# Kernel optimization log

Measured on AMD Instinct MI355X. Metric: run time of the kernel, lower is better.

The kernel has to match this reference:

```python
import jax, jax.numpy as jnp
import numpy as np

B, S, D, H, HD = 2, 2048, 2048, 16, 128
MAX_TIMESCALE = 10000.0


def _fixed_pos_embedding(features, length, max_timescale):
    # flaxformer embedding.generate_fixed_pos_embedding
    fraction = jnp.arange(0, features, 2, dtype=jnp.float32) / features
    timescale = max_timescale ** fraction  # min_timescale = 1.0
    sinusoid = jnp.einsum('i,j->ij', jnp.arange(length, dtype=jnp.float32), 1.0 / timescale)
    sinusoid = jnp.concatenate([sinusoid, sinusoid], axis=-1)  # [length, features]
    return jnp.sin(sinusoid), jnp.cos(sinusoid)


def _rotate_half(x):
    x1, x2 = jnp.split(x, 2, axis=-1)
    return jnp.concatenate([-x2, x1], axis=-1)


def _apply_rope(x, sin, cos):
    # x: [B, S, H, HD]; sin/cos: [S, HD]
    sin = sin[None, :, None, :].astype(x.dtype)
    cos = cos[None, :, None, :].astype(x.dtype)
    return x * cos + _rotate_half(x) * sin


def setup_inputs() -> dict:
    key = jax.random.key(0)
    ks = jax.random.split(key, 6)
    inputs_q = jax.random.normal(ks[0], (B, S, D), dtype=jnp.float32)
    inputs_kv = jax.random.normal(ks[1], (B, S, D), dtype=jnp.float32)
    scale = D ** -0.5
    wq = jax.random.normal(ks[2], (D, H, HD), dtype=jnp.float32) * scale
    wk = jax.random.normal(ks[3], (D, H, HD), dtype=jnp.float32) * scale
    wv = jax.random.normal(ks[4], (D, H, HD), dtype=jnp.float32) * scale
    wo = jax.random.normal(ks[5], (H, HD, D), dtype=jnp.float32) * ((H * HD) ** -0.5)
    mask = jnp.tril(jnp.ones((S, S), dtype=bool))[None, None]  # causal [1,1,S,S]
    return {"inputs_q": inputs_q, "inputs_kv": inputs_kv, "wq": wq, "wk": wk,
            "wv": wv, "wo": wo, "mask": mask}


def reference(inputs_q, inputs_kv, wq, wk, wv, wo, mask):
    # QKV projections (split-head kernels) -> [B, S, H, HD]
    q = jnp.einsum('bqd,dhf->bqhf', inputs_q, wq)
    k = jnp.einsum('bkd,dhf->bkhf', inputs_kv, wk)
    v = jnp.einsum('bkd,dhf->bkhf', inputs_kv, wv)

    # Rotary embeddings applied to full head dim (fraction_to_rotate = 1.0)
    sin, cos = _fixed_pos_embedding(HD, S, MAX_TIMESCALE)
    q = _apply_rope(q, sin, cos)
    k = _apply_rope(k, sin, cos)

    # Logit rescaling by 1/sqrt(head_dim) (rescale_logits=False default path)
    q = q * (HD ** -0.5)

    logits = jnp.einsum('bqhf,bkhf->bhqk', q, k)  # [B, H, S, S]
    logits = jnp.where(mask, logits, jnp.asarray(-1e10, logits.dtype))
    probs = jax.nn.softmax(logits, axis=-1)

    ctx = jnp.einsum('bhqk,bkhf->bqhf', probs, v)
    out = jnp.einsum('bqhf,hfd->bqd', ctx, wo)  # output projection
    return out
```

## Files before the change

kernel.cpp:

```cpp
#include <hip/hip_runtime.h>

#define S_LEN 2048
#define NH 16
#define HDIM 128
#define DMODEL 2048

typedef __attribute__((ext_vector_type(8))) short bf16x8;
typedef __attribute__((ext_vector_type(4))) float f32x4;

using gas_cvp = const __attribute__((address_space(1))) void*;
using las_vp  = __attribute__((address_space(3))) void*;

__device__ __forceinline__ unsigned short f2bf(float x) {
  unsigned int u = __builtin_bit_cast(unsigned int, x);
  u += 0x7FFFu + ((u >> 16) & 1u);
  return (unsigned short)(u >> 16);
}
__device__ __forceinline__ float bf2f(unsigned short u) {
  unsigned int x = ((unsigned int)u) << 16;
  return __builtin_bit_cast(float, x);
}
__device__ __forceinline__ unsigned int cvt_pk_bf16(float lo, float hi) {
  unsigned int r;
  asm("v_cvt_pk_bf16_f32 %0, %1, %2" : "=v"(r) : "v"(lo), "v"(hi));
  return r;
}

__global__ __launch_bounds__(256) void cvt_kernel(const float4* __restrict__ in,
                                                  ushort4* __restrict__ out, int n4) {
  int i = blockIdx.x * 256 + threadIdx.x;
  if (i < n4) {
    float4 v = in[i];
    ushort4 r;
    r.x = f2bf(v.x); r.y = f2bf(v.y); r.z = f2bf(v.z); r.w = f2bf(v.w);
    out[i] = r;
  }
}

__global__ __launch_bounds__(256) void sincos_kernel(float2* __restrict__ sc) {
  int i = blockIdx.x * 256 + threadIdx.x;
  int s = i >> 6, j = i & 63;
  float inv_ts = 1.0f / powf(10000.0f, (float)j * (1.0f / 64.0f));
  float ang = (float)s * inv_ts;
  sc[i] = make_float2(sinf(ang), cosf(ang));
}

__global__ __launch_bounds__(256) void rope8_kernel(const unsigned short* __restrict__ XQ,
                                                    const unsigned short* __restrict__ XK,
                                                    const float2* __restrict__ sc,
                                                    unsigned short* __restrict__ outQ,
                                                    unsigned short* __restrict__ outK,
                                                    float qscale) {
  const unsigned short* X = blockIdx.z ? XK : XQ;
  unsigned short* out = blockIdx.z ? outK : outQ;
  float scale = blockIdx.z ? 1.0f : qscale;
  int i = blockIdx.x * 256 + threadIdx.x;
  int m = i >> 7;
  int r = i & 127;
  int h = r >> 3, jb = (r & 7) * 8;
  int s = m & (S_LEN - 1);
  size_t base = (size_t)m * DMODEL + h * HDIM + jb;
  int4 x1 = *(const int4*)(X + base);
  int4 x2 = *(const int4*)(X + base + 64);
  const float2* pp = sc + s * 64 + jb;
  int4 o1, o2;
  int* x1w = (int*)&x1; int* x2w = (int*)&x2;
  int* o1w = (int*)&o1; int* o2w = (int*)&o2;
#pragma unroll
  for (int w = 0; w < 4; w++) {
    float a_lo = bf2f((unsigned short)(x1w[w] & 0xffff));
    float a_hi = bf2f((unsigned short)((unsigned int)x1w[w] >> 16));
    float b_lo = bf2f((unsigned short)(x2w[w] & 0xffff));
    float b_hi = bf2f((unsigned short)((unsigned int)x2w[w] >> 16));
    float2 c0 = pp[w * 2], c1 = pp[w * 2 + 1];
    float r1l = (a_lo * c0.y - b_lo * c0.x) * scale;
    float r1h = (a_hi * c1.y - b_hi * c1.x) * scale;
    float r2l = (b_lo * c0.y + a_lo * c0.x) * scale;
    float r2h = (b_hi * c1.y + a_hi * c1.x) * scale;
    o1w[w] = (int)(cvt_pk_bf16(r1l, r1h));
    o2w[w] = (int)(cvt_pk_bf16(r2l, r2h));
  }
  *(int4*)(out + base) = o1;
  *(int4*)(out + base + 64) = o2;
}

__global__ __launch_bounds__(256) void wtrans4_kernel(const float* __restrict__ w0,
                                                      const float* __restrict__ w1,
                                                      const float* __restrict__ w2,
                                                      const float* __restrict__ w3,
                                                      unsigned short* __restrict__ outb) {
  __shared__ float tile[64][65];
  int z = blockIdx.z;
  const float* in = (z == 0) ? w0 : (z == 1) ? w1 : (z == 2) ? w2 : w3;
  unsigned short* out = outb + (size_t)z * DMODEL * DMODEL;
  int c0 = blockIdx.x * 64, r0 = blockIdx.y * 64;
  int tx = threadIdx.x & 63, ty = threadIdx.x >> 6;
#pragma unroll
  for (int i = 0; i < 16; i++) {
    int r = ty + i * 4;
    tile[r][tx] = in[(size_t)(r0 + r) * DMODEL + c0 + tx];
  }
  __syncthreads();
#pragma unroll
  for (int i = 0; i < 16; i++) {
    int c = ty + i * 4;
    out[(size_t)(c0 + c) * DMODEL + r0 + tx] = f2bf(tile[tx][c]);
  }
}

__global__ __launch_bounds__(256) void vtrans_kernel(const unsigned short* __restrict__ vf,
                                                     unsigned short* __restrict__ Vt) {
  __shared__ unsigned short tile[64][65];
  int z = blockIdx.z; int b = z >> 4, h = z & 15;
  const unsigned short* I = vf + (size_t)b * S_LEN * DMODEL + h * HDIM;
  unsigned short* O = Vt + (size_t)z * HDIM * S_LEN;
  int s0 = blockIdx.y * 64, f0 = blockIdx.x * 64;
  int tx = threadIdx.x & 63, ty = threadIdx.x >> 6;
#pragma unroll
  for (int i = 0; i < 16; i++) {
    int r = ty + i * 4;
    tile[r][tx] = I[(size_t)(s0 + r) * DMODEL + f0 + tx];
  }
  __syncthreads();
#pragma unroll
  for (int i = 0; i < 16; i++) {
    int c = ty + i * 4;
    O[(size_t)(f0 + c) * S_LEN + s0 + tx] = tile[tx][c];
  }
}

template <bool BF16OUT>
__global__ __launch_bounds__(512, 1) void gemmk_kernel(
    const unsigned short* __restrict__ Aq,
    const unsigned short* __restrict__ Akv,
    const unsigned short* __restrict__ W,
    void* __restrict__ Cb) {
  constexpr int M = 4096, N = 2048, K = 2048, NT = K / 64;
  __shared__ char lds[147456];
  int z = blockIdx.z;
  const unsigned short* A = (z == 0) ? Aq : Akv;
  const unsigned short* Bt = W + (size_t)z * N * K;

  int wid = blockIdx.y * 16 + blockIdx.x;
  int nid = (wid & 7) * 32 + (wid >> 3);
  int bn = (nid & 15) * 128, bm = (nid >> 4) * 256;

  int tid = threadIdx.x, wave = tid >> 6, lane = tid & 63;
  int lr = lane & 15, lq = lane >> 4;
  int wr = wave >> 1, wc = wave & 1;

  auto STAGE_U = [&](int t, int buf, int which) {
    int k0 = t * 64;
    const unsigned short* src = (which < 2) ? A : Bt;
    int rbase = (which < 2) ? (bm + which * 128) : bn;
    char* dst0 = lds + buf * 49152 + which * 16384;
#pragma unroll
    for (int i = 0; i < 2; i++) {
      int o = i * 8192 + wave * 1024 + lane * 16;
      int row = o >> 7, colb = o & 127;
      int sc = colb ^ ((row & 7) << 4);
      __builtin_amdgcn_global_load_lds(
          (gas_cvp)(src + (size_t)(rbase + row) * K + k0 + (sc >> 1)),
          (las_vp)(dst0 + i * 8192 + wave * 1024), 16, 0, 0);
    }
  };
  auto LDA = [&](int buf, int m, int kk) -> bf16x8 {
    int row = wr * 64 + m * 16 + lr;
    int half = row >> 7, r = row & 127;
    int byt = r * 128 + (((kk * 4 + lq) ^ (r & 7)) << 4);
    return *(const bf16x8*)(lds + buf * 49152 + half * 16384 + byt);
  };
  auto LDB = [&](int buf, int n, int kk) -> bf16x8 {
    int row = wc * 64 + n * 16 + lr;
    int byt = row * 128 + (((kk * 4 + lq) ^ (row & 7)) << 4);
    return *(const bf16x8*)(lds + buf * 49152 + 32768 + byt);
  };

  f32x4 acc[4][4] = {};
  bf16x8 aA[4][2], bB[4][2];

  auto QUAD = [&](int mg, int ng) {
#pragma unroll
    for (int kk = 0; kk < 2; kk++)
#pragma unroll
      for (int mm = 0; mm < 2; mm++)
#pragma unroll
        for (int nn = 0; nn < 2; nn++)
          acc[mg * 2 + mm][ng * 2 + nn] = __builtin_amdgcn_mfma_f32_16x16x32_bf16(
              aA[mg * 2 + mm][kk], bB[ng * 2 + nn][kk], acc[mg * 2 + mm][ng * 2 + nn], 0, 0, 0);
  };

  auto BODY = [&](int T, int cur, int dst, int mode) {
    __builtin_amdgcn_s_barrier();
    if (mode == 0) {
      STAGE_U(T + 2, dst, 0); STAGE_U(T + 2, dst, 1); STAGE_U(T + 2, dst, 2);
    }
    __builtin_amdgcn_sched_barrier(0);
#pragma unroll
    for (int kk = 0; kk < 2; kk++)
#pragma unroll
      for (int mm = 0; mm < 2; mm++) aA[mm][kk] = LDA(cur, mm, kk);
#pragma unroll
    for (int kk = 0; kk < 2; kk++)
#pragma unroll
      for (int nn = 0; nn < 2; nn++) bB[nn][kk] = LDB(cur, nn, kk);
    __builtin_amdgcn_sched_barrier(0);
#pragma unroll
    for (int kk = 0; kk < 2; kk++)
#pragma unroll
      for (int nn = 0; nn < 2; nn++) bB[2 + nn][kk] = LDB(cur, 2 + nn, kk);
    __builtin_amdgcn_sched_barrier(0);
#pragma unroll
    for (int kk = 0; kk < 2; kk++)
#pragma unroll
      for (int mm = 0; mm < 2; mm++) aA[2 + mm][kk] = LDA(cur, 2 + mm, kk);
    __builtin_amdgcn_sched_barrier(0);

    asm volatile("s_waitcnt lgkmcnt(8)" ::: "memory");
    __builtin_amdgcn_sched_barrier(0);
    __builtin_amdgcn_s_setprio(1);
    QUAD(0, 0);
    __builtin_amdgcn_s_setprio(0);
    asm volatile("s_waitcnt lgkmcnt(4)" ::: "memory");
    __builtin_amdgcn_sched_barrier(0);
    __builtin_amdgcn_s_setprio(1);
    QUAD(0, 1);
    __builtin_amdgcn_s_setprio(0);
    asm volatile("s_waitcnt lgkmcnt(0)" ::: "memory");
    __builtin_amdgcn_sched_barrier(0);
    __builtin_amdgcn_s_setprio(1);
    QUAD(1, 0); QUAD(1, 1);
    __builtin_amdgcn_s_setprio(0);
    if (mode == 0)      asm volatile("s_waitcnt vmcnt(6)" ::: "memory");
    else if (mode == 1) asm volatile("s_waitcnt vmcnt(0)" ::: "memory");
    __builtin_amdgcn_sched_barrier(0);
  };

  STAGE_U(0, 0, 0); STAGE_U(0, 0, 1); STAGE_U(0, 0, 2);
  STAGE_U(1, 1, 0); STAGE_U(1, 1, 1); STAGE_U(1, 1, 2);
  asm volatile("s_waitcnt vmcnt(6)" ::: "memory");
  __builtin_amdgcn_sched_barrier(0);

  int cur = 0;
  for (int T = 0; T < NT - 2; T++) {
    int dst = (cur == 0) ? 2 : cur - 1;
    BODY(T, cur, dst, 0);
    cur = (cur == 2) ? 0 : cur + 1;
  }
  BODY(NT - 2, cur, 0, 1);
  cur = (cur == 2) ? 0 : cur + 1;
  BODY(NT - 1, cur, 0, 2);
  asm volatile("s_waitcnt vmcnt(0) lgkmcnt(0)" ::: "memory");

#pragma unroll
  for (int m = 0; m < 4; m++)
#pragma unroll
    for (int n = 0; n < 4; n++) {
      int row0 = bm + wr * 64 + m * 16 + lq * 4;
      int col = bn + wc * 64 + n * 16 + lr;
      if (BF16OUT) {
        unsigned short* C = (unsigned short*)Cb + (size_t)z * M * N;
#pragma unroll
        for (int r = 0; r < 4; r++)
          C[(size_t)(row0 + r) * N + col] = f2bf(acc[m][n][r]);
      } else {
        float* C = (float*)Cb + (size_t)z * M * N;
#pragma unroll
        for (int r = 0; r < 4; r++)
          C[(size_t)(row0 + r) * N + col] = acc[m][n][r];
      }
    }
}

__global__ __launch_bounds__(512, 1) void attn_kernel(const unsigned short* __restrict__ Qb,
                                                      const unsigned short* __restrict__ Kb,
                                                      const unsigned short* __restrict__ Vt,
                                                      unsigned short* __restrict__ ctx) {
  __shared__ char lds[65536];
  int d = blockIdx.x + 8 * (blockIdx.y + 16 * blockIdx.z);
  int jlo = (d >> 3) & 7;
  int hb = (d & 7) * 4 + (d >> 6);
  int h = hb & 15, b = hb >> 4;

  int tid = threadIdx.x, wave = tid >> 6, lane = tid & 63;
  int lr = lane & 15, lq = lane >> 4;
  int grp = wave >> 2, wsub = wave & 3;
  int qtile = grp ? (15 - jlo) : jlo;
  int qw = qtile * 128 + wsub * 32;
  int nt = 2 * (15 - jlo) + 2;

  const unsigned short* Qp = Qb + (size_t)b * S_LEN * DMODEL + (size_t)h * HDIM;
  const unsigned short* Kp = Kb + (size_t)b * S_LEN * DMODEL + (size_t)h * HDIM;
  const unsigned short* Vp = Vt + (size_t)(b * NH + h) * HDIM * S_LEN;

  bf16x8 qa[2][4];
#pragma unroll
  for (int mi = 0; mi < 2; mi++)
#pragma unroll
    for (int kf = 0; kf < 4; kf++)
      qa[mi][kf] = *(const bf16x8*)(Qp + (size_t)(qw + mi * 16 + lr) * DMODEL + kf * 32 + lq * 8);

  f32x4 o[2][8] = {};
  float mrow[2] = {-1e30f, -1e30f};
  float lsum[2] = {0.f, 0.f};

  auto STAGE = [&](int tt, int bsel) {
    int kk0 = tt * 64;
#pragma unroll
    for (int i = 0; i < 2; i++) {
      int o_ = wave * 2048 + i * 1024 + lane * 16;
      int row = o_ >> 8, colb = o_ & 255;
      int sc_ = colb ^ ((row & 7) << 4);
      __builtin_amdgcn_global_load_lds(
          (gas_cvp)(Kp + (size_t)(kk0 + row) * DMODEL + (sc_ >> 1)),
          (las_vp)(lds + bsel * 32768 + wave * 2048 + i * 1024), 16, 0, 0);
    }
#pragma unroll
    for (int i = 0; i < 2; i++) {
      int o_ = wave * 2048 + i * 1024 + lane * 16;
      int row = o_ >> 7, colb = o_ & 127;
      int sc_ = colb ^ ((row & 7) << 4);
      __builtin_amdgcn_global_load_lds(
          (gas_cvp)(Vp + (size_t)row * S_LEN + kk0 + (sc_ >> 1)),
          (las_vp)(lds + bsel * 32768 + 16384 + wave * 2048 + i * 1024), 16, 0, 0);
    }
  };

  STAGE(0, 0);
  __syncthreads();

  for (int t = 0; t < nt; t++) {
    int cur = t & 1;
    int k0 = t * 64;
    if (t + 1 < nt) STAGE(t + 1, cur ^ 1);

    bool active = (k0 <= qw + 31);
    if (active) {
      const char* kbb = lds + cur * 32768;
      f32x4 sf[2][4] = {};
#pragma unroll
      for (int kf = 0; kf < 4; kf++) {
        bf16x8 kbf[4];
#pragma unroll
        for (int nf = 0; nf < 4; nf++) {
          int row = nf * 16 + lr;
          int colb = kf * 64 + lq * 16;
          kbf[nf] = *(const bf16x8*)(kbb + row * 256 + (colb ^ ((row & 7) << 4)));
        }
#pragma unroll
        for (int nf = 0; nf < 4; nf++)
#pragma unroll
          for (int mi = 0; mi < 2; mi++)
            sf[mi][nf] = __builtin_amdgcn_mfma_f32_16x16x32_bf16(kbf[nf], qa[mi][kf], sf[mi][nf], 0, 0, 0);
      }

      if (k0 + 63 > qw) {
#pragma unroll
        for (int mi = 0; mi < 2; mi++) {
          int q = qw + mi * 16 + lr;
#pragma unroll
          for (int nf = 0; nf < 4; nf++)
#pragma unroll
            for (int r = 0; r < 4; r++)
              if (k0 + nf * 16 + lq * 4 + r > q) sf[mi][nf][r] = -1e30f;
        }
      }

      float vmax[2];
#pragma unroll
      for (int mi = 0; mi < 2; mi++) {
        float v = sf[mi][0][0];
#pragma unroll
        for (int nf = 0; nf < 4; nf++)
#pragma unroll
          for (int r = 0; r < 4; r++) v = fmaxf(v, sf[mi][nf][r]);
        v = fmaxf(v, __shfl_xor(v, 16));
        v = fmaxf(v, __shfl_xor(v, 32));
        vmax[mi] = v;
      }
      bool need = (vmax[0] > mrow[0] + 8.f) || (vmax[1] > mrow[1] + 8.f);
      if (__any(need)) {
#pragma unroll
        for (int mi = 0; mi < 2; mi++) {
          float mn = fmaxf(mrow[mi], vmax[mi]);
          float al = __expf(mrow[mi] - mn);
          mrow[mi] = mn;
          lsum[mi] *= al;
#pragma unroll
          for (int ff = 0; ff < 8; ff++) o[mi][ff] *= al;
        }
      }
#pragma unroll
      for (int mi = 0; mi < 2; mi++) {
        float rs = 0.f;
#pragma unroll
        for (int nf = 0; nf < 4; nf++)
#pragma unroll
          for (int r = 0; r < 4; r++) {
            float p = __expf(sf[mi][nf][r] - mrow[mi]);
            sf[mi][nf][r] = p;
            rs += p;
          }
        rs += __shfl_xor(rs, 16);
        rs += __shfl_xor(rs, 32);
        lsum[mi] += rs;
      }

      const char* vbb = lds + cur * 32768 + 16384;
      bool hi = (lane >= 32);
      bool odd = (lq & 1);
#pragma unroll
      for (int c = 0; c < 2; c++) {
        bf16x8 pfrag[2];
#pragma unroll
        for (int mi = 0; mi < 2; mi++) {
          unsigned int A0 = cvt_pk_bf16(sf[mi][2 * c][0], sf[mi][2 * c][1]);
          unsigned int A1 = cvt_pk_bf16(sf[mi][2 * c][2], sf[mi][2 * c][3]);
          unsigned int B0 = cvt_pk_bf16(sf[mi][2 * c + 1][0], sf[mi][2 * c + 1][1]);
          unsigned int B1 = cvt_pk_bf16(sf[mi][2 * c + 1][2], sf[mi][2 * c + 1][3]);
          unsigned int sA0 = (unsigned int)__shfl_xor((int)A0, 32);
          unsigned int sA1 = (unsigned int)__shfl_xor((int)A1, 32);
          unsigned int sB0 = (unsigned int)__shfl_xor((int)B0, 32);
          unsigned int sB1 = (unsigned int)__shfl_xor((int)B1, 32);
          unsigned int Y0f = hi ? sB0 : A0, Y0s = hi ? B0 : sA0;
          unsigned int Y1f = hi ? sB1 : A1, Y1s = hi ? B1 : sA1;
          unsigned int z0 = odd ? Y0f : Y0s, z1 = odd ? Y1f : Y1s;
          unsigned int w0 = (unsigned int)__shfl_xor((int)z0, 16);
          unsigned int w1 = (unsigned int)__shfl_xor((int)z1, 16);
          int4 fr;
          fr.x = (int)(odd ? w0 : Y0f);
          fr.y = (int)(odd ? w1 : Y1f);
          fr.z = (int)(odd ? Y0s : w0);
          fr.w = (int)(odd ? Y1s : w1);
          pfrag[mi] = __builtin_bit_cast(bf16x8, fr);
        }
#pragma unroll
        for (int ff = 0; ff < 8; ff++) {
          int row = ff * 16 + lr;
          int colb = c * 64 + lq * 16;
          bf16x8 vb = *(const bf16x8*)(vbb + row * 128 + (colb ^ ((row & 7) << 4)));
#pragma unroll
          for (int mi = 0; mi < 2; mi++)
            o[mi][ff] = __builtin_amdgcn_mfma_f32_16x16x32_bf16(vb, pfrag[mi], o[mi][ff], 0, 0, 0);
        }
      }
    }

    __syncthreads();
  }

#pragma unroll
  for (int mi = 0; mi < 2; mi++) {
    float inv = 1.0f / lsum[mi];
    size_t rb = ((size_t)b * S_LEN + qw + mi * 16 + lr) * DMODEL + h * HDIM;
#pragma unroll
    for (int ff = 0; ff < 8; ff++) {
      unsigned int u0 = cvt_pk_bf16(o[mi][ff][0] * inv, o[mi][ff][1] * inv);
      unsigned int u1 = cvt_pk_bf16(o[mi][ff][2] * inv, o[mi][ff][3] * inv);
      *(uint2*)(ctx + rb + ff * 16 + lq * 4) = make_uint2(u0, u1);
    }
  }
}

extern "C" void kernel_launch(void* const* d_in, const int* in_sizes, int n_in,
                              void* d_out, int out_size, void* d_ws, size_t ws_size,
                              hipStream_t stream) {
  const float* inq  = (const float*)d_in[0];
  const float* inkv = (const float*)d_in[1];
  const float* wq   = (const float*)d_in[2];
  const float* wk   = (const float*)d_in[3];
  const float* wv   = (const float*)d_in[4];
  const float* wo   = (const float*)d_in[5];
  float* out = (float*)d_out;

  char* ws = (char*)d_ws;
  const size_t MB = 1ull << 20;
  unsigned short* xq  = (unsigned short*)(ws);
  unsigned short* xkv = (unsigned short*)(ws + 16 * MB);
  unsigned short* wqt = (unsigned short*)(ws + 32 * MB);
  unsigned short* wot = (unsigned short*)(ws + 56 * MB);
  float2* sc          = (float2*)(ws + 64 * MB);
  unsigned short* projb = (unsigned short*)(ws + 66 * MB);
  unsigned short* Vt   = (unsigned short*)(ws + 114 * MB);
  unsigned short* ctxb = (unsigned short*)(ws + 130 * MB);
  unsigned short* Qb = xq;
  unsigned short* Kb = xkv;

  const int n4 = (2 * S_LEN * DMODEL) / 4;
  cvt_kernel<<<n4 / 256, 256, 0, stream>>>((const float4*)inq, (ushort4*)xq, n4);
  cvt_kernel<<<n4 / 256, 256, 0, stream>>>((const float4*)inkv, (ushort4*)xkv, n4);

  wtrans4_kernel<<<dim3(32, 32, 4), 256, 0, stream>>>(wq, wk, wv, wo, wqt);

  sincos_kernel<<<(S_LEN * 64) / 256, 256, 0, stream>>>(sc);

  const float qscale = 0.08838834764831845f;
  unsigned short* projQ = projb;
  unsigned short* projK = projb + (size_t)4096 * 2048;
  unsigned short* projV = projb + (size_t)2 * 4096 * 2048;

  gemmk_kernel<true><<<dim3(16, 16, 3), 512, 0, stream>>>(xq, xkv, wqt, (void*)projb);

  rope8_kernel<<<dim3(2048, 1, 2), 256, 0, stream>>>(projQ, projK, sc, Qb, Kb, qscale);
  vtrans_kernel<<<dim3(2, 32, 32), 256, 0, stream>>>(projV, Vt);

  attn_kernel<<<dim3(8, NH, 2), 512, 0, stream>>>(Qb, Kb, Vt, ctxb);

  gemmk_kernel<false><<<dim3(16, 16, 1), 512, 0, stream>>>(ctxb, ctxb, wot, (void*)out);
}
```

Baseline: 283.9 us.

## Use 256x256-tile GEMM for Q/K projections and merge input conversion launches

Adds a new projection GEMM kernel with 256x256 output tiles, double-buffered LDS staging, interleaved LDS reads and MFMA groups, and priority hints. It computes the Q and K projections, while V keeps the old 256x128 kernel in a separate launch. The larger tile raises arithmetic intensity per staged byte, but it is double- rather than triple-buffered and the Q/K grid is only 256 blocks. The two float-to-bf16 conversion launches are also merged into one using the z grid dimension.

```diff
diff --git a/kernel.cpp b/kernel.cpp
--- a/kernel.cpp
+++ b/kernel.cpp
@@ -26,8 +26,12 @@
   return r;
 }
 
-__global__ __launch_bounds__(256) void cvt_kernel(const float4* __restrict__ in,
-                                                  ushort4* __restrict__ out, int n4) {
+__global__ __launch_bounds__(256) void cvt2_kernel(const float4* __restrict__ inq,
+                                                   const float4* __restrict__ inkv,
+                                                   ushort4* __restrict__ outq,
+                                                   ushort4* __restrict__ outkv, int n4) {
+  const float4* in = blockIdx.z ? inkv : inq;
+  ushort4* out = blockIdx.z ? outkv : outq;
   int i = blockIdx.x * 256 + threadIdx.x;
   if (i < n4) {
     float4 v = in[i];
@@ -129,6 +133,144 @@
   }
 }
 
+__global__ __launch_bounds__(512, 1) void gemm256o_kernel(
+    const unsigned short* __restrict__ Aq,
+    const unsigned short* __restrict__ Akv,
+    const unsigned short* __restrict__ W,
+    unsigned short* __restrict__ Cb) {
+  constexpr int M = 4096, N = 2048, K = 2048, NT = K / 64;
+  __shared__ char lds[131072];
+  int wid = blockIdx.z * 128 + blockIdx.y * 8 + blockIdx.x;
+  int nid = (wid & 7) * 32 + (wid >> 3);
+  int z = nid >> 7;
+  int rem = nid & 127;
+  int bm = (rem >> 3) * 256, bn = (rem & 7) * 256;
+  const unsigned short* A = (z == 0) ? Aq : Akv;
+  const unsigned short* Bt = W + (size_t)z * N * K;
+
+  int tid = threadIdx.x, wave = tid >> 6, lane = tid & 63;
+  int lr = lane & 15, lq = lane >> 4;
+  int wr = wave >> 2, wc = wave & 3;
+
+  auto STAGE_P = [&](int t, int buf, int isB) {
+    int k0 = t * 64;
+    const unsigned short* src = isB ? Bt : A;
+    int rbase = isB ? bn : bm;
+    char* dst0 = lds + buf * 65536 + isB * 32768;
+#pragma unroll
+    for (int i = 0; i < 4; i++) {
+      int o = i * 8192 + tid * 16;
+      int row = o >> 7, colb = o & 127;
+      int sc = colb ^ ((row & 7) << 4);
+      __builtin_amdgcn_global_load_lds(
+          (gas_cvp)(src + (size_t)(rbase + row) * K + k0 + (sc >> 1)),
+          (las_vp)(dst0 + i * 8192 + wave * 1024), 16, 0, 0);
+    }
+  };
+  auto LDA1 = [&](int buf, int m, int kk) -> bf16x8 {
+    int row = wr * 128 + m * 16 + lr;
+    return *(const bf16x8*)(lds + buf * 65536 + row * 128 +
+                            (((kk * 4 + lq) ^ (row & 7)) << 4));
+  };
+  auto LDB1 = [&](int buf, int n, int kk) -> bf16x8 {
+    int row = wc * 64 + n * 16 + lr;
+    return *(const bf16x8*)(lds + buf * 65536 + 32768 + row * 128 +
+                            (((kk * 4 + lq) ^ (row & 7)) << 4));
+  };
+
+  f32x4 acc[8][4] = {};
+  bf16x8 aA[4][2], bB[4][2];
+
+  auto OCT = [&](int P, int Q, int sb) {
+#pragma unroll
+    for (int kk = 0; kk < 2; kk++)
+#pragma unroll
+      for (int s = 0; s < 2; s++)
+#pragma unroll
+        for (int nn = 0; nn < 2; nn++)
+          acc[2 * P + s][2 * Q + nn] = __builtin_amdgcn_mfma_f32_16x16x32_bf16(
+              aA[sb + s][kk], bB[2 * Q + nn][kk], acc[2 * P + s][2 * Q + nn], 0, 0, 0);
+  };
+  auto RD_A2 = [&](int buf, int m0, int sb) {
+#pragma unroll
+    for (int kk = 0; kk < 2; kk++)
+#pragma unroll
+      for (int s = 0; s < 2; s++) aA[sb + s][kk] = LDA1(buf, m0 + s, kk);
+  };
+  auto RD_B2 = [&](int buf, int n0) {
+#pragma unroll
+    for (int kk = 0; kk < 2; kk++)
+#pragma unroll
+      for (int s = 0; s < 2; s++) bB[n0 + s][kk] = LDB1(buf, n0 + s, kk);
+  };
+
+  STAGE_P(0, 0, 0); STAGE_P(0, 0, 1);
+  asm volatile("s_waitcnt vmcnt(0)" ::: "memory");
+  __builtin_amdgcn_sched_barrier(0);
+
+  for (int T = 0; T < NT; T++) {
+    int c = T & 1, nc = c ^ 1;
+    __builtin_amdgcn_s_barrier();
+    if (T + 1 < NT) { STAGE_P(T + 1, nc, 0); STAGE_P(T + 1, nc, 1); }
+    __builtin_amdgcn_sched_barrier(0);
+    RD_A2(c, 0, 0);
+    __builtin_amdgcn_sched_barrier(0);
+    RD_B2(c, 0);
+    __builtin_amdgcn_sched_barrier(0);
+    RD_B2(c, 2);
+    __builtin_amdgcn_sched_barrier(0);
+    RD_A2(c, 2, 2);
+    __builtin_amdgcn_sched_barrier(0);
+
+    asm volatile("s_waitcnt lgkmcnt(8)" ::: "memory");
+    __builtin_amdgcn_sched_barrier(0);
+    __builtin_amdgcn_s_setprio(1);
+    OCT(0, 0, 0);
+    __builtin_amdgcn_s_setprio(0);
+    asm volatile("s_waitcnt lgkmcnt(4)" ::: "memory");
+    __builtin_amdgcn_sched_barrier(0);
+    __builtin_amdgcn_s_setprio(1);
+    OCT(0, 1, 0);
+    __builtin_amdgcn_s_setprio(0);
+    RD_A2(c, 4, 0);
+    __builtin_amdgcn_sched_barrier(0);
+    asm volatile("s_waitcnt lgkmcnt(4)" ::: "memory");
+    __builtin_amdgcn_sched_barrier(0);
+    __builtin_amdgcn_s_setprio(1);
+    OCT(1, 0, 2); OCT(1, 1, 2);
+    __builtin_amdgcn_s_setprio(0);
+    RD_A2(c, 6, 2);
+    __builtin_amdgcn_sched_barrier(0);
+    asm volatile("s_waitcnt lgkmcnt(4)" ::: "memory");
+    __builtin_amdgcn_sched_barrier(0);
+    __builtin_amdgcn_s_setprio(1);
+    OCT(2, 0, 0); OCT(2, 1, 0);
+    __builtin_amdgcn_s_setprio(0);
+    asm volatile("s_waitcnt lgkmcnt(0)" ::: "memory");
+    __builtin_amdgcn_sched_barrier(0);
+    __builtin_amdgcn_s_setprio(1);
+    OCT(3, 0, 2); OCT(3, 1, 2);
+    __builtin_amdgcn_s_setprio(0);
+    if (T + 1 < NT) {
+      asm volatile("s_waitcnt vmcnt(0)" ::: "memory");
+      __builtin_amdgcn_sched_barrier(0);
+    }
+  }
+  asm volatile("s_waitcnt vmcnt(0) lgkmcnt(0)" ::: "memory");
+
+  unsigned short* C = Cb + (size_t)z * M * N;
+#pragma unroll
+  for (int m = 0; m < 8; m++)
+#pragma unroll
+    for (int n = 0; n < 4; n++) {
+      int row0 = bm + wr * 128 + m * 16 + lq * 4;
+      int col = bn + wc * 64 + n * 16 + lr;
+#pragma unroll
+      for (int r = 0; r < 4; r++)
+        C[(size_t)(row0 + r) * N + col] = f2bf(acc[m][n][r]);
+    }
+}
+
 template <bool BF16OUT>
 __global__ __launch_bounds__(512, 1) void gemmk_kernel(
     const unsigned short* __restrict__ Aq,
@@ -259,12 +401,12 @@
       int row0 = bm + wr * 64 + m * 16 + lq * 4;
       int col = bn + wc * 64 + n * 16 + lr;
       if (BF16OUT) {
-        unsigned short* C = (unsigned short*)Cb + (size_t)z * M * N;
+        unsigned short* C = (unsigned short*)Cb;
 #pragma unroll
         for (int r = 0; r < 4; r++)
           C[(size_t)(row0 + r) * N + col] = f2bf(acc[m][n][r]);
       } else {
-        float* C = (float*)Cb + (size_t)z * M * N;
+        float* C = (float*)Cb;
 #pragma unroll
         for (int r = 0; r < 4; r++)
           C[(size_t)(row0 + r) * N + col] = acc[m][n][r];
@@ -478,6 +620,7 @@
   unsigned short* xq  = (unsigned short*)(ws);
   unsigned short* xkv = (unsigned short*)(ws + 16 * MB);
   unsigned short* wqt = (unsigned short*)(ws + 32 * MB);
+  unsigned short* wvt = (unsigned short*)(ws + 48 * MB);
   unsigned short* wot = (unsigned short*)(ws + 56 * MB);
   float2* sc          = (float2*)(ws + 64 * MB);
   unsigned short* projb = (unsigned short*)(ws + 66 * MB);
@@ -487,8 +630,8 @@
   unsigned short* Kb = xkv;
 
   const int n4 = (2 * S_LEN * DMODEL) / 4;
-  cvt_kernel<<<n4 / 256, 256, 0, stream>>>((const float4*)inq, (ushort4*)xq, n4);
-  cvt_kernel<<<n4 / 256, 256, 0, stream>>>((const float4*)inkv, (ushort4*)xkv, n4);
+  cvt2_kernel<<<dim3(n4 / 256, 1, 2), 256, 0, stream>>>(
+      (const float4*)inq, (const float4*)inkv, (ushort4*)xq, (ushort4*)xkv, n4);
 
   wtrans4_kernel<<<dim3(32, 32, 4), 256, 0, stream>>>(wq, wk, wv, wo, wqt);
 
@@ -499,7 +642,8 @@
   unsigned short* projK = projb + (size_t)4096 * 2048;
   unsigned short* projV = projb + (size_t)2 * 4096 * 2048;
 
-  gemmk_kernel<true><<<dim3(16, 16, 3), 512, 0, stream>>>(xq, xkv, wqt, (void*)projb);
+  gemm256o_kernel<<<dim3(8, 16, 2), 512, 0, stream>>>(xq, xkv, wqt, projb);
+  gemmk_kernel<true><<<dim3(16, 16, 1), 512, 0, stream>>>(xkv, xkv, wvt, (void*)projV);
 
   rope8_kernel<<<dim3(2048, 1, 2), 256, 0, stream>>>(projQ, projK, sc, Qb, Kb, qscale);
   vtrans_kernel<<<dim3(2, 32, 32), 256, 0, stream>>>(projV, Vt);
```

Result: faster. 264.3 us (-6.9%).
